# Optimization experiments

Measured on AMD Instinct MI355X. Metric: run time of the kernel, lower is better.

Reference implementation:

```python
import jax, jax.numpy as jnp
import numpy as np

B = 4
N0, N1, N2 = 32768, 8192, 2048
C0, C1, C2 = 256, 512, 1024
EPS = 1e-5  # torch BatchNorm1d default eps


def _mlp(x, w1, b1, g, be, w2, b2):
    # Linear -> BatchNorm1d (training-mode batch stats over B and N) -> ReLU -> Linear
    h = x @ w1 + b1                      # (B, N, H)
    mu = jnp.mean(h, axis=(0, 1))
    var = jnp.mean((h - mu) ** 2, axis=(0, 1))  # biased var, as torch BN uses for normalization
    h = jax.nn.relu((h - mu) * jax.lax.rsqrt(var + EPS) * g + be)
    return h @ w2 + b2


def _gather(feats, idx):
    # feats: (B, N_coarse, C), idx: (B, N_fine) -> (B, N_fine, C)
    return jax.vmap(lambda f, i: f[i])(feats, idx)


def _lin(key, fan_in, fan_out, scale=0.02):
    return jax.random.normal(key, (fan_in, fan_out), dtype=jnp.float32) * scale


def setup_inputs() -> dict:
    key = jax.random.key(0)
    ks = jax.random.split(key, 16)
    inp = {
        'f0': jax.random.normal(ks[0], (B, N0, C0), dtype=jnp.float32),
        'f1': jax.random.normal(ks[1], (B, N1, C1), dtype=jnp.float32),
        'f2': jax.random.normal(ks[2], (B, N2, C2), dtype=jnp.float32),
        # up_mlps[0]: MLP(C1, [C1, C0])
        'up0_w1': _lin(ks[3], C1, C1), 'up0_b1': jnp.zeros((C1,), jnp.float32),
        'up0_g': jnp.ones((C1,), jnp.float32), 'up0_be': jnp.zeros((C1,), jnp.float32),
        'up0_w2': _lin(ks[4], C1, C0), 'up0_b2': jnp.zeros((C0,), jnp.float32),
        # up_mlps[1]: MLP(C2, [C2, C1])
        'up1_w1': _lin(ks[5], C2, C2), 'up1_b1': jnp.zeros((C2,), jnp.float32),
        'up1_g': jnp.ones((C2,), jnp.float32), 'up1_be': jnp.zeros((C2,), jnp.float32),
        'up1_w2': _lin(ks[6], C2, C1), 'up1_b2': jnp.zeros((C1,), jnp.float32),
        # skip_mlps[0]: MLP(2*C0, [2*C0, C0])
        'skip0_w1': _lin(ks[7], 2 * C0, 2 * C0), 'skip0_b1': jnp.zeros((2 * C0,), jnp.float32),
        'skip0_g': jnp.ones((2 * C0,), jnp.float32), 'skip0_be': jnp.zeros((2 * C0,), jnp.float32),
        'skip0_w2': _lin(ks[8], 2 * C0, C0), 'skip0_b2': jnp.zeros((C0,), jnp.float32),
        # skip_mlps[1]: MLP(2*C1, [2*C1, C1])
        'skip1_w1': _lin(ks[9], 2 * C1, 2 * C1), 'skip1_b1': jnp.zeros((2 * C1,), jnp.float32),
        'skip1_g': jnp.ones((2 * C1,), jnp.float32), 'skip1_be': jnp.zeros((2 * C1,), jnp.float32),
        'skip1_w2': _lin(ks[10], 2 * C1, C1), 'skip1_b2': jnp.zeros((C1,), jnp.float32),
        'pool0': jax.random.randint(ks[11], (B, N0), 0, N1, dtype=jnp.int32),
        'pool1': jax.random.randint(ks[12], (B, N1), 0, N2, dtype=jnp.int32),
    }
    return inp


def reference(f0, f1, f2,
              up0_w1, up0_b1, up0_g, up0_be, up0_w2, up0_b2,
              up1_w1, up1_b1, up1_g, up1_be, up1_w2, up1_b2,
              skip0_w1, skip0_b1, skip0_g, skip0_be, skip0_w2, skip0_b2,
              skip1_w1, skip1_b1, skip1_g, skip1_be, skip1_w2, skip1_b2,
              pool0, pool1):
    # start at coarsest level
    x = f2                                               # (B, N2, C2)
    # level i = 1
    x = _mlp(x, up1_w1, up1_b1, up1_g, up1_be, up1_w2, up1_b2)   # (B, N2, C1)
    x = _gather(x, pool1)                                 # (B, N1, C1)
    x = _mlp(jnp.concatenate([f1, x], axis=-1),
             skip1_w1, skip1_b1, skip1_g, skip1_be, skip1_w2, skip1_b2)  # (B, N1, C1)
    # level i = 0
    x = _mlp(x, up0_w1, up0_b1, up0_g, up0_be, up0_w2, up0_b2)   # (B, N1, C0)
    x = _gather(x, pool0)                                 # (B, N0, C0)
    x = _mlp(jnp.concatenate([f0, x], axis=-1),
             skip0_w1, skip0_b1, skip0_g, skip0_be, skip0_w2, skip0_b2)  # (B, N0, C0)
    return x
```

## Files before the change

kernel.cpp:

```cpp
#include <hip/hip_runtime.h>


typedef unsigned short u16;
typedef __attribute__((ext_vector_type(8))) short bf16x8;
typedef __attribute__((ext_vector_type(4))) float f32x4;

#define UNROLL _Pragma("unroll")
#define EPW 136

__device__ __forceinline__ float b2f(u16 u) {
    union { unsigned int i; float f; } v; v.i = ((unsigned int)u) << 16; return v.f;
}
__device__ __forceinline__ u16 f2b(float f) {
    union { float f; unsigned int i; } v; v.f = f;
    unsigned int r = v.i + 0x7FFFu + ((v.i >> 16) & 1u);
    return (u16)(r >> 16);
}

__device__ __forceinline__ void gld_lds16(const u16* g, u16* l) {
    __builtin_amdgcn_global_load_lds(
        (const __attribute__((address_space(1))) unsigned int*)g,
        (__attribute__((address_space(3))) unsigned int*)l,
        16, 0, 0);
}

#define VMCNT(n) asm volatile("s_waitcnt vmcnt(" #n ")" ::: "memory")
#define LGKM0    asm volatile("s_waitcnt lgkmcnt(0)" ::: "memory")
#define BAR()    do{ asm volatile("" ::: "memory"); \
                     __builtin_amdgcn_s_barrier(); \
                     asm volatile("" ::: "memory"); }while(0)

union SMem {
    struct { u16 a[3][16384]; u16 b[2][8192]; } g;
    struct { u16 a[2][16384]; u16 b[2][8192]; float ss[2048]; } f;
    u16 ep[256 * EPW];
};

template <bool AFFINE_A, bool STATS, bool OUT_F32, bool GATHER>
__global__ __launch_bounds__(1024, 4) void gemm_bn(
    const u16* __restrict__ A, const u16* __restrict__ BT, void* __restrict__ Cout,
    const float* __restrict__ scale, const float* __restrict__ shift,
    const float* __restrict__ bias,
    float* __restrict__ psum, float* __restrict__ psumsq,
    const u16* __restrict__ Xg, const int* __restrict__ pool,
    int nfShift, int Nc, int Chalf,
    int N, int K)
{
    __shared__ __align__(16) SMem sm;

    const int tid  = threadIdx.x;
    const int w    = tid >> 6;
    const int lane = tid & 63;
    const int wm   = w >> 2, wn = w & 3;
    const int l15  = lane & 15;
    const int xorv = (lane & 7) << 3;
    const int swz8 = ((lane & 7) ^ (lane >> 3)) << 3;
    const int kS0  = ((lane >> 4) << 3) ^ xorv;
    const int kS1  = (32 + ((lane >> 4) << 3)) ^ xorv;

    int bm, bn;
    {
        const int nbn  = (int)gridDim.x;
        const int nwg  = nbn * (int)gridDim.y;
        const int flat = (int)(blockIdx.y * gridDim.x + blockIdx.x);
        const int wg   = (flat & 7) * (nwg >> 3) + (flat >> 3);
        const int lb   = 31 - __builtin_clz(nbn);
        bn = wg & (nbn - 1);
        bm = wg >> lb;
    }

    const u16* aS[2]; const u16* xS[2]; const u16* bSp;
    int dA[2], dB, wIdx[2];
    UNROLL for (int u = 0; u < 2; u++) {
        const int trb = (w >> 2) * 64 + (w & 3) * 8 + u * 32;
        const int tr  = trb + (lane >> 3);
        dA[u] = trb * 64;
        const int rowG = bm * 256 + tr;
        if constexpr (GATHER) {
            const int b = rowG >> nfShift;
            const int p = pool[rowG];
            aS[u] = A  + (size_t)rowG * Chalf + swz8;
            xS[u] = Xg + ((size_t)b * Nc + p) * Chalf + swz8;
        } else if constexpr (AFFINE_A) {
            aS[u] = A + (size_t)rowG * K + ((lane & 7) << 3);
            wIdx[u] = tr * 64 + swz8;
        } else {
            aS[u] = A + (size_t)rowG * K + swz8;
        }
    }
    {
        const int trb = w * 8;
        dB = trb * 64;
        bSp = BT + (size_t)(bn * 128 + trb + (lane >> 3)) * K + swz8;
    }

    f32x4 acc[4][2];
    const f32x4 zero = {0.f, 0.f, 0.f, 0.f};
    UNROLL for (int i = 0; i < 4; i++)
    UNROLL for (int j = 0; j < 2; j++) acc[i][j] = zero;
    bf16x8 afr[2][2];
    bf16x8 bfr[2][2];
    uint4 rA[2];

#define GLD_B(BASE, KOF) gld_lds16(bSp + (KOF), (BASE) + dB)

#define ISSUE_A(u, BASE, KOF) do{ \
    if constexpr (GATHER) { \
        const u16* s_ = ((KOF) < Chalf) ? (aS[u] + (KOF)) : (xS[u] + ((KOF) - Chalf)); \
        gld_lds16(s_, (BASE) + dA[u]); \
    } else { \
        gld_lds16(aS[u] + (KOF), (BASE) + dA[u]); \
    } }while(0)

#define LOAD_RA(u, KOF) do{ rA[u] = *(const uint4*)(aS[u] + (KOF)); }while(0)

#define AFFW(u, BASE, KOF) do{ if constexpr (AFFINE_A) { \
    const int kb_ = (KOF) + ((lane & 7) << 3); \
    const float4 sc0_ = *(const float4*)&sm.f.ss[kb_]; \
    const float4 sc1_ = *(const float4*)&sm.f.ss[kb_ + 4]; \
    const float4 sh0_ = *(const float4*)&sm.f.ss[1024 + kb_]; \
    const float4 sh1_ = *(const float4*)&sm.f.ss[1024 + kb_ + 4]; \
    union { uint4 u4; u16 s[8]; } r_, o_; r_.u4 = rA[u]; \
    o_.s[0] = f2b(fmaxf(b2f(r_.s[0]) * sc0_.x + sh0_.x, 0.f)); \
    o_.s[1] = f2b(fmaxf(b2f(r_.s[1]) * sc0_.y + sh0_.y, 0.f)); \
    o_.s[2] = f2b(fmaxf(b2f(r_.s[2]) * sc0_.z + sh0_.z, 0.f)); \
    o_.s[3] = f2b(fmaxf(b2f(r_.s[3]) * sc0_.w + sh0_.w, 0.f)); \
    o_.s[4] = f2b(fmaxf(b2f(r_.s[4]) * sc1_.x + sh1_.x, 0.f)); \
    o_.s[5] = f2b(fmaxf(b2f(r_.s[5]) * sc1_.y + sh1_.y, 0.f)); \
    o_.s[6] = f2b(fmaxf(b2f(r_.s[6]) * sc1_.z + sh1_.z, 0.f)); \
    o_.s[7] = f2b(fmaxf(b2f(r_.s[7]) * sc1_.w + sh1_.w, 0.f)); \
    *(uint4*)&((BASE))[wIdx[u]] = o_.u4; \
    LGKM0; } }while(0)

#define READ_A(base, qi) do{ const u16* p_ = (base); \
    UNROLL for (int i2 = 0; i2 < 2; i2++) { \
        const int rb_ = (wm * 64 + ((qi) * 2 + i2) * 16 + l15) * 64; \
        afr[i2][0] = *(const bf16x8*)&p_[rb_ + kS0]; \
        afr[i2][1] = *(const bf16x8*)&p_[rb_ + kS1]; } }while(0)

#define READ_B(base) do{ const u16* p_ = (base); \
    UNROLL for (int j_ = 0; j_ < 2; j_++) { \
        const int rb_ = (wn * 32 + j_ * 16 + l15) * 64; \
        bfr[j_][0] = *(const bf16x8*)&p_[rb_ + kS0]; \
        bfr[j_][1] = *(const bf16x8*)&p_[rb_ + kS1]; } }while(0)

#define MFMA_PH(qi) do{ __builtin_amdgcn_s_setprio(1); \
    UNROLL for (int i2 = 0; i2 < 2; i2++) \
    UNROLL for (int j_ = 0; j_ < 2; j_++) { \
        acc[(qi)*2+i2][j_] = __builtin_amdgcn_mfma_f32_16x16x32_bf16( \
            afr[i2][0], bfr[j_][0], acc[(qi)*2+i2][j_], 0, 0, 0); \
        acc[(qi)*2+i2][j_] = __builtin_amdgcn_mfma_f32_16x16x32_bf16( \
            afr[i2][1], bfr[j_][1], acc[(qi)*2+i2][j_], 0, 0, 0); } \
    __builtin_amdgcn_s_setprio(0); }while(0)

    const int nkt = K >> 6;

    if constexpr (AFFINE_A) {
        for (int i = tid; i < K; i += 1024) {
            sm.f.ss[i] = scale[i]; sm.f.ss[1024 + i] = shift[i];
        }
        LOAD_RA(0, 0); LOAD_RA(1, 0);
        GLD_B(&sm.f.b[0][0], 0);
        GLD_B(&sm.f.b[1][0], 64);
        LGKM0;
        BAR();
        AFFW(0, &sm.f.a[0][0], 0);
        LOAD_RA(0, 64);
        VMCNT(2);
        BAR();

        for (int t = 0; t < nkt - 2; ++t) {
            u16* aB = &sm.f.a[t & 1][0]; u16* aN = &sm.f.a[(t + 1) & 1][0];
            u16* bR = &sm.f.b[t & 1][0];
            const int kofN = (t + 1) << 6, kof2 = (t + 2) << 6;
            AFFW(1, aB, t << 6);
            LOAD_RA(1, kofN);
            READ_A(aB, 0); READ_B(bR);
            LGKM0; BAR();
            MFMA_PH(0);
            AFFW(0, aN, kofN);
            LOAD_RA(0, kof2);
            GLD_B(bR, kof2);
            READ_A(aB, 1);
            LGKM0; VMCNT(3);
            BAR();
            MFMA_PH(1);
        }
        {
            const int t = nkt - 2;
            u16* aB = &sm.f.a[t & 1][0]; u16* aN = &sm.f.a[(t + 1) & 1][0];
            u16* bR = &sm.f.b[t & 1][0];
            const int kofN = (t + 1) << 6;
            AFFW(1, aB, t << 6); LOAD_RA(1, kofN);
            READ_A(aB, 0); READ_B(bR);
            LGKM0; BAR();
            MFMA_PH(0);
            AFFW(0, aN, kofN);
            READ_A(aB, 1);
            LGKM0; VMCNT(1);
            BAR();
            MFMA_PH(1);
        }
        {
            const int t = nkt - 1;
            u16* aB = &sm.f.a[t & 1][0]; u16* bR = &sm.f.b[t & 1][0];
            AFFW(1, aB, t << 6);
            READ_A(aB, 0); READ_B(bR);
            LGKM0; BAR();
            MFMA_PH(0);
            READ_A(aB, 1);
            LGKM0; BAR();
            MFMA_PH(1);
        }
    } else {
        GLD_B(&sm.g.b[0][0], 0);
        GLD_B(&sm.g.b[1][0], 64);
        ISSUE_A(0, &sm.g.a[0][0], 0);  ISSUE_A(1, &sm.g.a[0][0], 0);
        ISSUE_A(0, &sm.g.a[1][0], 64); ISSUE_A(1, &sm.g.a[1][0], 64);
        VMCNT(0); BAR();

        int rs = 0;
        for (int t = 0; t < nkt - 2; ++t) {
            const int ws = (rs >= 1) ? rs - 1 : 2;
            u16* aR = &sm.g.a[0][0] + rs * 16384;
            u16* aW = &sm.g.a[0][0] + ws * 16384;
            u16* bR = &sm.g.b[t & 1][0];
            const int kof2 = (t + 2) << 6;
            ISSUE_A(0, aW, kof2);
            READ_A(aR, 0); READ_B(bR);
            LGKM0; BAR();
            MFMA_PH(0);
            ISSUE_A(1, aW, kof2);
            GLD_B(bR, kof2);
            READ_A(aR, 1);
            LGKM0; VMCNT(3);
            BAR();
            MFMA_PH(1);
            rs = (rs == 2) ? 0 : rs + 1;
        }
        {
            u16* aR = &sm.g.a[0][0] + rs * 16384;
            u16* bR = &sm.g.b[(nkt - 2) & 1][0];
            READ_A(aR, 0); READ_B(bR);
            LGKM0; BAR();
            MFMA_PH(0);
            READ_A(aR, 1);
            LGKM0; VMCNT(0);
            BAR();
            MFMA_PH(1);
            rs = (rs == 2) ? 0 : rs + 1;
        }
        {
            u16* aR = &sm.g.a[0][0] + rs * 16384;
            u16* bR = &sm.g.b[(nkt - 1) & 1][0];
            READ_A(aR, 0); READ_B(bR);
            LGKM0; BAR();
            MFMA_PH(0);
            READ_A(aR, 1);
            LGKM0; BAR();
            MFMA_PH(1);
        }
    }

    const int cl = l15, quad = lane >> 4;
    if constexpr (OUT_F32) {
        UNROLL for (int j = 0; j < 2; j++) {
            const int col = bn * 128 + wn * 32 + j * 16 + cl;
            const float bcol = bias[col];
            UNROLL for (int i = 0; i < 4; i++) {
                const int r0 = bm * 256 + wm * 64 + i * 16 + quad * 4;
                UNROLL for (int r = 0; r < 4; r++)
                    ((float*)Cout)[(size_t)(r0 + r) * N + col] = acc[i][j][r] + bcol;
            }
        }
    } else {
        UNROLL for (int j = 0; j < 2; j++) {
            const int colL = wn * 32 + j * 16 + cl;
            const int col = bn * 128 + colL;
            float bcol = 0.f;
            if constexpr (!STATS) bcol = bias[col];
            float s = 0.f, ss2 = 0.f;
            UNROLL for (int i = 0; i < 4; i++) {
                const int rL0 = wm * 64 + i * 16 + quad * 4;
                UNROLL for (int r = 0; r < 4; r++) {
                    const float v = acc[i][j][r];
                    if constexpr (STATS) { s += v; ss2 += v * v; }
                    sm.ep[(rL0 + r) * EPW + colL] = f2b(v + bcol);
                }
            }
            if constexpr (STATS) {
                s   += __shfl_xor(s, 16);   s   += __shfl_xor(s, 32);
                ss2 += __shfl_xor(ss2, 16); ss2 += __shfl_xor(ss2, 32);
                if (quad == 0) { atomicAdd(&psum[col], s); atomicAdd(&psumsq[col], ss2); }
            }
        }
        __syncthreads();
        u16* Cb = (u16*)Cout;
        UNROLL for (int it = 0; it < 4; it++) {
            const int row = it * 64 + (tid >> 4);
            const int c8  = (tid & 15) * 8;
            const uint4 v = *(const uint4*)&sm.ep[row * EPW + c8];
            *(uint4*)(Cb + (size_t)(bm * 256 + row) * N + bn * 128 + c8) = v;
        }
    }
#undef GLD_B
#undef ISSUE_A
#undef LOAD_RA
#undef AFFW
#undef READ_A
#undef READ_B
#undef MFMA_PH
}

__global__ void cvt_transpose_w(const float* __restrict__ W, u16* __restrict__ WT, int K, int N) {
    __shared__ float t[32][33];
    const int tx = threadIdx.x, ty = threadIdx.y;
    const int n0 = blockIdx.x * 32, k0 = blockIdx.y * 32;
#pragma unroll
    for (int r = 0; r < 4; r++)
        t[ty + r * 8][tx] = W[(size_t)(k0 + ty + r * 8) * N + n0 + tx];
    __syncthreads();
#pragma unroll
    for (int r = 0; r < 4; r++)
        WT[(size_t)(n0 + ty + r * 8) * K + k0 + tx] = f2b(t[tx][ty + r * 8]);
}

__global__ void cvt_f32_bf16(const float* __restrict__ x, u16* __restrict__ y, long n8) {
    const long t = (long)blockIdx.x * 256 + threadIdx.x;
    if (t >= n8) return;
    const float4 a = ((const float4*)x)[t * 2];
    const float4 b = ((const float4*)x)[t * 2 + 1];
    union { uint4 u; u16 s[8]; } o;
    o.s[0] = f2b(a.x); o.s[1] = f2b(a.y); o.s[2] = f2b(a.z); o.s[3] = f2b(a.w);
    o.s[4] = f2b(b.x); o.s[5] = f2b(b.y); o.s[6] = f2b(b.z); o.s[7] = f2b(b.w);
    ((uint4*)y)[t] = o.u;
}

__global__ void bn_finalize(const float* __restrict__ sum, const float* __restrict__ sumsq,
                            const float* __restrict__ g, const float* __restrict__ be,
                            float* __restrict__ scale, float* __restrict__ shift,
                            int Cc, float invM) {
    const int c = blockIdx.x * 256 + threadIdx.x;
    if (c >= Cc) return;
    const float mu = sum[c] * invM;
    const float var = fmaf(sumsq[c], invM, -mu * mu);
    const float sc = g[c] * rsqrtf(var + 1e-5f);
    scale[c] = sc;
    shift[c] = fmaf(-mu, sc, be[c]);
}

extern "C" void kernel_launch(void* const* d_in, const int* in_sizes, int n_in,
                              void* d_out, int out_size, void* d_ws, size_t ws_size,
                              hipStream_t stream) {
    const float* f0     = (const float*)d_in[0];
    const float* f1     = (const float*)d_in[1];
    const float* f2     = (const float*)d_in[2];
    const float* up0_w1 = (const float*)d_in[3];
    const float* up0_g  = (const float*)d_in[5];
    const float* up0_be = (const float*)d_in[6];
    const float* up0_w2 = (const float*)d_in[7];
    const float* up0_b2 = (const float*)d_in[8];
    const float* up1_w1 = (const float*)d_in[9];
    const float* up1_g  = (const float*)d_in[11];
    const float* up1_be = (const float*)d_in[12];
    const float* up1_w2 = (const float*)d_in[13];
    const float* up1_b2 = (const float*)d_in[14];
    const float* sk0_w1 = (const float*)d_in[15];
    const float* sk0_g  = (const float*)d_in[17];
    const float* sk0_be = (const float*)d_in[18];
    const float* sk0_w2 = (const float*)d_in[19];
    const float* sk0_b2 = (const float*)d_in[20];
    const float* sk1_w1 = (const float*)d_in[21];
    const float* sk1_g  = (const float*)d_in[23];
    const float* sk1_be = (const float*)d_in[24];
    const float* sk1_w2 = (const float*)d_in[25];
    const float* sk1_b2 = (const float*)d_in[26];
    const int* pool0    = (const int*)d_in[27];
    const int* pool1    = (const int*)d_in[28];
    float* out = (float*)d_out;

    char* ws = (char*)d_ws;
    size_t off = 0;
    auto alloc = [&](size_t bytes) -> void* {
        void* p = ws + off;
        off += (bytes + 255) & ~(size_t)255;
        return p;
    };
    u16* w_up1_1 = (u16*)alloc((size_t)1024 * 1024 * 2);
    u16* w_up1_2 = (u16*)alloc((size_t)512 * 1024 * 2);
    u16* w_sk1_1 = (u16*)alloc((size_t)1024 * 1024 * 2);
    u16* w_sk1_2 = (u16*)alloc((size_t)512 * 1024 * 2);
    u16* w_up0_1 = (u16*)alloc((size_t)512 * 512 * 2);
    u16* w_up0_2 = (u16*)alloc((size_t)256 * 512 * 2);
    u16* w_sk0_1 = (u16*)alloc((size_t)512 * 512 * 2);
    u16* w_sk0_2 = (u16*)alloc((size_t)256 * 512 * 2);
    float* stats = (float*)alloc((size_t)4 * 4096 * 4);
    u16* Hbuf    = (u16*)alloc((size_t)131072 * 512 * 2);
    u16* Xbuf    = (u16*)alloc((size_t)32768 * 512 * 2);
    u16* f0b     = (u16*)alloc((size_t)4 * 32768 * 256 * 2);
    u16* f1b     = (u16*)alloc((size_t)4 * 8192 * 512 * 2);
    u16* f2b_    = (u16*)alloc((size_t)4 * 2048 * 1024 * 2);

    const dim3 tb(32, 8);
    cvt_transpose_w<<<dim3(32, 32), tb, 0, stream>>>(up1_w1, w_up1_1, 1024, 1024);
    cvt_transpose_w<<<dim3(16, 32), tb, 0, stream>>>(up1_w2, w_up1_2, 1024, 512);
    cvt_transpose_w<<<dim3(32, 32), tb, 0, stream>>>(sk1_w1, w_sk1_1, 1024, 1024);
    cvt_transpose_w<<<dim3(16, 32), tb, 0, stream>>>(sk1_w2, w_sk1_2, 1024, 512);
    cvt_transpose_w<<<dim3(16, 16), tb, 0, stream>>>(up0_w1, w_up0_1, 512, 512);
    cvt_transpose_w<<<dim3(8, 16),  tb, 0, stream>>>(up0_w2, w_up0_2, 512, 256);
    cvt_transpose_w<<<dim3(16, 16), tb, 0, stream>>>(sk0_w1, w_sk0_1, 512, 512);
    cvt_transpose_w<<<dim3(8, 16),  tb, 0, stream>>>(sk0_w2, w_sk0_2, 512, 256);

    hipMemsetAsync(stats, 0, (size_t)4 * 4096 * sizeof(float), stream);
    cvt_f32_bf16<<<4096,  256, 0, stream>>>(f2, f2b_, 8388608L / 8);
    cvt_f32_bf16<<<8192,  256, 0, stream>>>(f1, f1b, 16777216L / 8);
    cvt_f32_bf16<<<16384, 256, 0, stream>>>(f0, f0b, 33554432L / 8);

    float* st0 = stats;
    float* st1 = stats + 4096;
    float* st2 = stats + 8192;
    float* st3 = stats + 12288;

    gemm_bn<false, true, false, false><<<dim3(8, 32), 1024, 0, stream>>>(
        f2b_, w_up1_1, Hbuf, nullptr, nullptr, nullptr, st0, st0 + 1024,
        nullptr, nullptr, 0, 0, 0, 1024, 1024);
    bn_finalize<<<4, 256, 0, stream>>>(st0, st0 + 1024, up1_g, up1_be, st0 + 2048, st0 + 3072, 1024, 1.f / 8192.f);
    gemm_bn<true, false, false, false><<<dim3(4, 32), 1024, 0, stream>>>(
        Hbuf, w_up1_2, Xbuf, st0 + 2048, st0 + 3072, up1_b2, nullptr, nullptr,
        nullptr, nullptr, 0, 0, 0, 512, 1024);

    gemm_bn<false, true, false, true><<<dim3(8, 128), 1024, 0, stream>>>(
        f1b, w_sk1_1, Hbuf, nullptr, nullptr, nullptr, st1, st1 + 1024,
        Xbuf, pool1, 13, 2048, 512, 1024, 1024);
    bn_finalize<<<4, 256, 0, stream>>>(st1, st1 + 1024, sk1_g, sk1_be, st1 + 2048, st1 + 3072, 1024, 1.f / 32768.f);
    gemm_bn<true, false, false, false><<<dim3(4, 128), 1024, 0, stream>>>(
        Hbuf, w_sk1_2, Xbuf, st1 + 2048, st1 + 3072, sk1_b2, nullptr, nullptr,
        nullptr, nullptr, 0, 0, 0, 512, 1024);

    gemm_bn<false, true, false, false><<<dim3(4, 128), 1024, 0, stream>>>(
        Xbuf, w_up0_1, Hbuf, nullptr, nullptr, nullptr, st2, st2 + 1024,
        nullptr, nullptr, 0, 0, 0, 512, 512);
    bn_finalize<<<2, 256, 0, stream>>>(st2, st2 + 1024, up0_g, up0_be, st2 + 2048, st2 + 3072, 512, 1.f / 32768.f);
    gemm_bn<true, false, false, false><<<dim3(2, 128), 1024, 0, stream>>>(
        Hbuf, w_up0_2, Xbuf, st2 + 2048, st2 + 3072, up0_b2, nullptr, nullptr,
        nullptr, nullptr, 0, 0, 0, 256, 512);

    gemm_bn<false, true, false, true><<<dim3(4, 512), 1024, 0, stream>>>(
        f0b, w_sk0_1, Hbuf, nullptr, nullptr, nullptr, st3, st3 + 1024,
        Xbuf, pool0, 15, 8192, 256, 512, 512);
    bn_finalize<<<2, 256, 0, stream>>>(st3, st3 + 1024, sk0_g, sk0_be, st3 + 2048, st3 + 3072, 512, 1.f / 131072.f);
    gemm_bn<true, false, true, false><<<dim3(2, 512), 1024, 0, stream>>>(
        Hbuf, w_sk0_2, out, st3 + 2048, st3 + 3072, sk0_b2, nullptr, nullptr,
        nullptr, nullptr, 0, 0, 0, 256, 512);
}
```

Baseline: 850.8 us.

## Shrink GEMM tile to 128x128 with 512 threads and simple double-buffered loop

Changes the fused GEMM+BN kernel from 256x128 tiles with 1024 threads and a hand-scheduled triple-buffered, split-phase pipeline to 128x128 tiles with 512 threads and a plain two-stage double buffer that prefetches the next k-tile while computing the current one. The smaller LDS footprint and block size are meant to allow more resident workgroups and more blocks per launch, hiding latency through occupancy rather than intra-block software pipelining. The trade-off is less operand reuse per tile, more global/B traffic, a full vmcnt(0) wait each iteration, and the loss of the finer-grained MFMA/load interleaving.

```diff
diff --git a/kernel.cpp b/kernel.cpp
--- a/kernel.cpp
+++ b/kernel.cpp
@@ -31,13 +31,12 @@
                      asm volatile("" ::: "memory"); }while(0)
 
 union SMem {
-    struct { u16 a[3][16384]; u16 b[2][8192]; } g;
-    struct { u16 a[2][16384]; u16 b[2][8192]; float ss[2048]; } f;
-    u16 ep[256 * EPW];
+    struct { u16 a[2][8192]; u16 b[2][8192]; float ss[2048]; } st;
+    u16 ep[128 * EPW];
 };
 
 template <bool AFFINE_A, bool STATS, bool OUT_F32, bool GATHER>
-__global__ __launch_bounds__(1024, 4) void gemm_bn(
+__global__ __launch_bounds__(512, 4) void gemm_bn(
     const u16* __restrict__ A, const u16* __restrict__ BT, void* __restrict__ Cout,
     const float* __restrict__ scale, const float* __restrict__ shift,
     const float* __restrict__ bias,
@@ -55,8 +54,6 @@
     const int l15  = lane & 15;
     const int xorv = (lane & 7) << 3;
     const int swz8 = ((lane & 7) ^ (lane >> 3)) << 3;
-    const int kS0  = ((lane >> 4) << 3) ^ xorv;
-    const int kS1  = (32 + ((lane >> 4) << 3)) ^ xorv;
 
     int bm, bn;
     {
@@ -69,13 +66,14 @@
         bm = wg >> lb;
     }
 
-    const u16* aS[2]; const u16* xS[2]; const u16* bSp;
-    int dA[2], dB, wIdx[2];
+    const u16* aS[2]; const u16* xS[2]; const u16* bS[2];
+    int dA[2], dB[2], wIdx[2];
     UNROLL for (int u = 0; u < 2; u++) {
-        const int trb = (w >> 2) * 64 + (w & 3) * 8 + u * 32;
+        const int trb = w * 16 + u * 8;
         const int tr  = trb + (lane >> 3);
         dA[u] = trb * 64;
-        const int rowG = bm * 256 + tr;
+        dB[u] = trb * 64;
+        const int rowG = bm * 128 + tr;
         if constexpr (GATHER) {
             const int b = rowG >> nfShift;
             const int p = pool[rowG];
@@ -87,22 +85,16 @@
         } else {
             aS[u] = A + (size_t)rowG * K + swz8;
         }
-    }
-    {
-        const int trb = w * 8;
-        dB = trb * 64;
-        bSp = BT + (size_t)(bn * 128 + trb + (lane >> 3)) * K + swz8;
+        bS[u] = BT + (size_t)(bn * 128 + tr) * K + swz8;
     }
 
     f32x4 acc[4][2];
     const f32x4 zero = {0.f, 0.f, 0.f, 0.f};
     UNROLL for (int i = 0; i < 4; i++)
     UNROLL for (int j = 0; j < 2; j++) acc[i][j] = zero;
-    bf16x8 afr[2][2];
-    bf16x8 bfr[2][2];
     uint4 rA[2];
 
-#define GLD_B(BASE, KOF) gld_lds16(bSp + (KOF), (BASE) + dB)
+#define GLD_B(u, BASE, KOF) gld_lds16(bS[u] + (KOF), (BASE) + dB[u])
 
 #define ISSUE_A(u, BASE, KOF) do{ \
     if constexpr (GATHER) { \
@@ -116,10 +108,10 @@
 
 #define AFFW(u, BASE, KOF) do{ if constexpr (AFFINE_A) { \
     const int kb_ = (KOF) + ((lane & 7) << 3); \
-    const float4 sc0_ = *(const float4*)&sm.f.ss[kb_]; \
-    const float4 sc1_ = *(const float4*)&sm.f.ss[kb_ + 4]; \
-    const float4 sh0_ = *(const float4*)&sm.f.ss[1024 + kb_]; \
-    const float4 sh1_ = *(const float4*)&sm.f.ss[1024 + kb_ + 4]; \
+    const float4 sc0_ = *(const float4*)&sm.st.ss[kb_]; \
+    const float4 sc1_ = *(const float4*)&sm.st.ss[kb_ + 4]; \
+    const float4 sh0_ = *(const float4*)&sm.st.ss[1024 + kb_]; \
+    const float4 sh1_ = *(const float4*)&sm.st.ss[1024 + kb_ + 4]; \
     union { uint4 u4; u16 s[8]; } r_, o_; r_.u4 = rA[u]; \
     o_.s[0] = f2b(fmaxf(b2f(r_.s[0]) * sc0_.x + sh0_.x, 0.f)); \
     o_.s[1] = f2b(fmaxf(b2f(r_.s[1]) * sc0_.y + sh0_.y, 0.f)); \
@@ -129,137 +121,63 @@
     o_.s[5] = f2b(fmaxf(b2f(r_.s[5]) * sc1_.y + sh1_.y, 0.f)); \
     o_.s[6] = f2b(fmaxf(b2f(r_.s[6]) * sc1_.z + sh1_.z, 0.f)); \
     o_.s[7] = f2b(fmaxf(b2f(r_.s[7]) * sc1_.w + sh1_.w, 0.f)); \
-    *(uint4*)&((BASE))[wIdx[u]] = o_.u4; \
-    LGKM0; } }while(0)
-
-#define READ_A(base, qi) do{ const u16* p_ = (base); \
-    UNROLL for (int i2 = 0; i2 < 2; i2++) { \
-        const int rb_ = (wm * 64 + ((qi) * 2 + i2) * 16 + l15) * 64; \
-        afr[i2][0] = *(const bf16x8*)&p_[rb_ + kS0]; \
-        afr[i2][1] = *(const bf16x8*)&p_[rb_ + kS1]; } }while(0)
-
-#define READ_B(base) do{ const u16* p_ = (base); \
-    UNROLL for (int j_ = 0; j_ < 2; j_++) { \
-        const int rb_ = (wn * 32 + j_ * 16 + l15) * 64; \
-        bfr[j_][0] = *(const bf16x8*)&p_[rb_ + kS0]; \
-        bfr[j_][1] = *(const bf16x8*)&p_[rb_ + kS1]; } }while(0)
-
-#define MFMA_PH(qi) do{ __builtin_amdgcn_s_setprio(1); \
-    UNROLL for (int i2 = 0; i2 < 2; i2++) \
-    UNROLL for (int j_ = 0; j_ < 2; j_++) { \
-        acc[(qi)*2+i2][j_] = __builtin_amdgcn_mfma_f32_16x16x32_bf16( \
-            afr[i2][0], bfr[j_][0], acc[(qi)*2+i2][j_], 0, 0, 0); \
-        acc[(qi)*2+i2][j_] = __builtin_amdgcn_mfma_f32_16x16x32_bf16( \
-            afr[i2][1], bfr[j_][1], acc[(qi)*2+i2][j_], 0, 0, 0); } \
-    __builtin_amdgcn_s_setprio(0); }while(0)
+    *(uint4*)&((BASE))[wIdx[u]] = o_.u4; } }while(0)
+
+#define COMPUTE_TILE(aB, bB) do{ \
+    UNROLL for (int ks = 0; ks < 2; ks++) { \
+        const int kS_ = (ks * 32 + ((lane >> 4) << 3)) ^ xorv; \
+        bf16x8 afr[4], bfr[2]; \
+        UNROLL for (int i_ = 0; i_ < 4; i_++) \
+            afr[i_] = *(const bf16x8*)&(aB)[(wm * 64 + i_ * 16 + l15) * 64 + kS_]; \
+        UNROLL for (int j_ = 0; j_ < 2; j_++) \
+            bfr[j_] = *(const bf16x8*)&(bB)[(wn * 32 + j_ * 16 + l15) * 64 + kS_]; \
+        __builtin_amdgcn_s_setprio(1); \
+        UNROLL for (int i_ = 0; i_ < 4; i_++) \
+        UNROLL for (int j_ = 0; j_ < 2; j_++) \
+            acc[i_][j_] = __builtin_amdgcn_mfma_f32_16x16x32_bf16( \
+                afr[i_], bfr[j_], acc[i_][j_], 0, 0, 0); \
+        __builtin_amdgcn_s_setprio(0); \
+    } }while(0)
 
     const int nkt = K >> 6;
 
     if constexpr (AFFINE_A) {
-        for (int i = tid; i < K; i += 1024) {
-            sm.f.ss[i] = scale[i]; sm.f.ss[1024 + i] = shift[i];
+        for (int i = tid; i < K; i += 512) {
+            sm.st.ss[i] = scale[i]; sm.st.ss[1024 + i] = shift[i];
         }
         LOAD_RA(0, 0); LOAD_RA(1, 0);
-        GLD_B(&sm.f.b[0][0], 0);
-        GLD_B(&sm.f.b[1][0], 64);
-        LGKM0;
-        BAR();
-        AFFW(0, &sm.f.a[0][0], 0);
-        LOAD_RA(0, 64);
-        VMCNT(2);
-        BAR();
-
-        for (int t = 0; t < nkt - 2; ++t) {
-            u16* aB = &sm.f.a[t & 1][0]; u16* aN = &sm.f.a[(t + 1) & 1][0];
-            u16* bR = &sm.f.b[t & 1][0];
-            const int kofN = (t + 1) << 6, kof2 = (t + 2) << 6;
-            AFFW(1, aB, t << 6);
-            LOAD_RA(1, kofN);
-            READ_A(aB, 0); READ_B(bR);
-            LGKM0; BAR();
-            MFMA_PH(0);
-            AFFW(0, aN, kofN);
-            LOAD_RA(0, kof2);
-            GLD_B(bR, kof2);
-            READ_A(aB, 1);
-            LGKM0; VMCNT(3);
-            BAR();
-            MFMA_PH(1);
-        }
-        {
-            const int t = nkt - 2;
-            u16* aB = &sm.f.a[t & 1][0]; u16* aN = &sm.f.a[(t + 1) & 1][0];
-            u16* bR = &sm.f.b[t & 1][0];
-            const int kofN = (t + 1) << 6;
-            AFFW(1, aB, t << 6); LOAD_RA(1, kofN);
-            READ_A(aB, 0); READ_B(bR);
-            LGKM0; BAR();
-            MFMA_PH(0);
-            AFFW(0, aN, kofN);
-            READ_A(aB, 1);
-            LGKM0; VMCNT(1);
-            BAR();
-            MFMA_PH(1);
-        }
-        {
-            const int t = nkt - 1;
-            u16* aB = &sm.f.a[t & 1][0]; u16* bR = &sm.f.b[t & 1][0];
-            AFFW(1, aB, t << 6);
-            READ_A(aB, 0); READ_B(bR);
-            LGKM0; BAR();
-            MFMA_PH(0);
-            READ_A(aB, 1);
-            LGKM0; BAR();
-            MFMA_PH(1);
-        }
+        GLD_B(0, &sm.st.b[0][0], 0); GLD_B(1, &sm.st.b[0][0], 0);
+        LGKM0; BAR();
+        AFFW(0, &sm.st.a[0][0], 0);
+        AFFW(1, &sm.st.a[0][0], 0);
+        VMCNT(0); LGKM0; BAR();
     } else {
-        GLD_B(&sm.g.b[0][0], 0);
-        GLD_B(&sm.g.b[1][0], 64);
-        ISSUE_A(0, &sm.g.a[0][0], 0);  ISSUE_A(1, &sm.g.a[0][0], 0);
-        ISSUE_A(0, &sm.g.a[1][0], 64); ISSUE_A(1, &sm.g.a[1][0], 64);
+        ISSUE_A(0, &sm.st.a[0][0], 0); ISSUE_A(1, &sm.st.a[0][0], 0);
+        GLD_B(0, &sm.st.b[0][0], 0);   GLD_B(1, &sm.st.b[0][0], 0);
         VMCNT(0); BAR();
-
-        int rs = 0;
-        for (int t = 0; t < nkt - 2; ++t) {
-            const int ws = (rs >= 1) ? rs - 1 : 2;
-            u16* aR = &sm.g.a[0][0] + rs * 16384;
-            u16* aW = &sm.g.a[0][0] + ws * 16384;
-            u16* bR = &sm.g.b[t & 1][0];
-            const int kof2 = (t + 2) << 6;
-            ISSUE_A(0, aW, kof2);
-            READ_A(aR, 0); READ_B(bR);
-            LGKM0; BAR();
-            MFMA_PH(0);
-            ISSUE_A(1, aW, kof2);
-            GLD_B(bR, kof2);
-            READ_A(aR, 1);
-            LGKM0; VMCNT(3);
-            BAR();
-            MFMA_PH(1);
-            rs = (rs == 2) ? 0 : rs + 1;
-        }
-        {
-            u16* aR = &sm.g.a[0][0] + rs * 16384;
-            u16* bR = &sm.g.b[(nkt - 2) & 1][0];
-            READ_A(aR, 0); READ_B(bR);
-            LGKM0; BAR();
-            MFMA_PH(0);
-            READ_A(aR, 1);
-            LGKM0; VMCNT(0);
-            BAR();
-            MFMA_PH(1);
-            rs = (rs == 2) ? 0 : rs + 1;
-        }
-        {
-            u16* aR = &sm.g.a[0][0] + rs * 16384;
-            u16* bR = &sm.g.b[(nkt - 1) & 1][0];
-            READ_A(aR, 0); READ_B(bR);
-            LGKM0; BAR();
-            MFMA_PH(0);
-            READ_A(aR, 1);
-            LGKM0; BAR();
-            MFMA_PH(1);
-        }
+    }
+
+    for (int t = 0; t < nkt; ++t) {
+        const int cb = t & 1, nb = cb ^ 1;
+        const int kofN = (t + 1) << 6;
+        u16* aC = &sm.st.a[cb][0]; u16* bC = &sm.st.b[cb][0];
+        u16* aN = &sm.st.a[nb][0]; u16* bN = &sm.st.b[nb][0];
+        const bool more = (t + 1 < nkt);
+        if (more) {
+            if constexpr (AFFINE_A) {
+                LOAD_RA(0, kofN); LOAD_RA(1, kofN);
+                GLD_B(0, bN, kofN); GLD_B(1, bN, kofN);
+            } else {
+                ISSUE_A(0, aN, kofN); ISSUE_A(1, aN, kofN);
+                GLD_B(0, bN, kofN); GLD_B(1, bN, kofN);
+            }
+        }
+        COMPUTE_TILE(aC, bC);
+        if (more) {
+            if constexpr (AFFINE_A) { AFFW(0, aN, kofN); AFFW(1, aN, kofN); }
+            VMCNT(0);
+        }
+        LGKM0; BAR();
     }
 
     const int cl = l15, quad = lane >> 4;
@@ -268,7 +186,7 @@
             const int col = bn * 128 + wn * 32 + j * 16 + cl;
             const float bcol = bias[col];
             UNROLL for (int i = 0; i < 4; i++) {
-                const int r0 = bm * 256 + wm * 64 + i * 16 + quad * 4;
+                const int r0 = bm * 128 + wm * 64 + i * 16 + quad * 4;
                 UNROLL for (int r = 0; r < 4; r++)
                     ((float*)Cout)[(size_t)(r0 + r) * N + col] = acc[i][j][r] + bcol;
             }
@@ -297,19 +215,17 @@
         __syncthreads();
         u16* Cb = (u16*)Cout;
         UNROLL for (int it = 0; it < 4; it++) {
-            const int row = it * 64 + (tid >> 4);
+            const int row = it * 32 + (tid >> 4);
             const int c8  = (tid & 15) * 8;
             const uint4 v = *(const uint4*)&sm.ep[row * EPW + c8];
-            *(uint4*)(Cb + (size_t)(bm * 256 + row) * N + bn * 128 + c8) = v;
+            *(uint4*)(Cb + (size_t)(bm * 128 + row) * N + bn * 128 + c8) = v;
         }
     }
 #undef GLD_B
 #undef ISSUE_A
 #undef LOAD_RA
 #undef AFFW
-#undef READ_A
-#undef READ_B
-#undef MFMA_PH
+#undef COMPUTE_TILE
 }
 
 __global__ void cvt_transpose_w(const float* __restrict__ W, u16* __restrict__ WT, int K, int N) {
@@ -421,35 +337,35 @@
     float* st2 = stats + 8192;
     float* st3 = stats + 12288;
 
-    gemm_bn<false, true, false, false><<<dim3(8, 32), 1024, 0, stream>>>(
+    gemm_bn<false, true, false, false><<<dim3(8, 64), 512, 0, stream>>>(
         f2b_, w_up1_1, Hbuf, nullptr, nullptr, nullptr, st0, st0 + 1024,
         nullptr, nullptr, 0, 0, 0, 1024, 1024);
     bn_finalize<<<4, 256, 0, stream>>>(st0, st0 + 1024, up1_g, up1_be, st0 + 2048, st0 + 3072, 1024, 1.f / 8192.f);
-    gemm_bn<true, false, false, false><<<dim3(4, 32), 1024, 0, stream>>>(
+    gemm_bn<true, false, false, false><<<dim3(4, 64), 512, 0, stream>>>(
         Hbuf, w_up1_2, Xbuf, st0 + 2048, st0 + 3072, up1_b2, nullptr, nullptr,
         nullptr, nullptr, 0, 0, 0, 512, 1024);
 
-    gemm_bn<false, true, false, true><<<dim3(8, 128), 1024, 0, stream>>>(
+    gemm_bn<false, true, false, true><<<dim3(8, 256), 512, 0, stream>>>(
         f1b, w_sk1_1, Hbuf, nullptr, nullptr, nullptr, st1, st1 + 1024,
         Xbuf, pool1, 13, 2048, 512, 1024, 1024);
     bn_finalize<<<4, 256, 0, stream>>>(st1, st1 + 1024, sk1_g, sk1_be, st1 + 2048, st1 + 3072, 1024, 1.f / 32768.f);
-    gemm_bn<true, false, false, false><<<dim3(4, 128), 1024, 0, stream>>>(
+    gemm_bn<true, false, false, false><<<dim3(4, 256), 512, 0, stream>>>(
         Hbuf, w_sk1_2, Xbuf, st1 + 2048, st1 + 3072, sk1_b2, nullptr, nullptr,
         nullptr, nullptr, 0, 0, 0, 512, 1024);
 
-    gemm_bn<false, true, false, false><<<dim3(4, 128), 1024, 0, stream>>>(
+    gemm_bn<false, true, false, false><<<dim3(4, 256), 512, 0, stream>>>(
         Xbuf, w_up0_1, Hbuf, nullptr, nullptr, nullptr, st2, st2 + 1024,
         nullptr, nullptr, 0, 0, 0, 512, 512);
     bn_finalize<<<2, 256, 0, stream>>>(st2, st2 + 1024, up0_g, up0_be, st2 + 2048, st2 + 3072, 512, 1.f / 32768.f);
-    gemm_bn<true, false, false, false><<<dim3(2, 128), 1024, 0, stream>>>(
+    gemm_bn<true, false, false, false><<<dim3(2, 256), 512, 0, stream>>>(
         Hbuf, w_up0_2, Xbuf, st2 + 2048, st2 + 3072, up0_b2, nullptr, nullptr,
         nullptr, nullptr, 0, 0, 0, 256, 512);
 
-    gemm_bn<false, true, false, true><<<dim3(4, 512), 1024, 0, stream>>>(
+    gemm_bn<false, true, false, true><<<dim3(4, 1024), 512, 0, stream>>>(
         f0b, w_sk0_1, Hbuf, nullptr, nullptr, nullptr, st3, st3 + 1024,
         Xbuf, pool0, 15, 8192, 256, 512, 512);
     bn_finalize<<<2, 256, 0, stream>>>(st3, st3 + 1024, sk0_g, sk0_be, st3 + 2048, st3 + 3072, 512, 1.f / 131072.f);
-    gemm_bn<true, false, true, false><<<dim3(2, 512), 1024, 0, stream>>>(
+    gemm_bn<true, false, true, false><<<dim3(2, 1024), 512, 0, stream>>>(
         Hbuf, w_sk0_2, out, st3 + 2048, st3 + 3072, sk0_b2, nullptr, nullptr,
         nullptr, nullptr, 0, 0, 0, 256, 512);
 }
```

New measurement: 864.8 us. No clear change (+1.6%).
